# Performance work log

Measured on AMD Instinct MI355X. Metric: run time of the kernel, lower is better.

Reference implementation:

```python
import jax, jax.numpy as jnp
import numpy as np
import math

EMBED_DIM = 2048
NUM_HEADS = 16
HEAD_DIM = EMBED_DIM // NUM_HEADS
BATCH = 4
SEQ = 2048


def setup_inputs() -> dict:
    key = jax.random.key(0)
    ks = jax.random.split(key, 5)
    scale_qkv = 1.0 / math.sqrt(EMBED_DIM)
    x = jax.random.normal(ks[0], (BATCH, SEQ, EMBED_DIM), dtype=jnp.float32)
    w_qkv = jax.random.normal(ks[1], (3 * EMBED_DIM, EMBED_DIM), dtype=jnp.float32) * scale_qkv
    b_qkv = jnp.zeros((3 * EMBED_DIM,), dtype=jnp.float32)
    w_o = jax.random.normal(ks[2], (EMBED_DIM, EMBED_DIM), dtype=jnp.float32) * scale_qkv
    b_o = jnp.zeros((EMBED_DIM,), dtype=jnp.float32)
    return {"x": x, "w_qkv": w_qkv, "b_qkv": b_qkv, "w_o": w_o, "b_o": b_o}


def reference(x, w_qkv, b_qkv, w_o, b_o):
    B, S, D = x.shape
    # fused QKV projection: [B,S,3D]
    qkv = jnp.einsum('bsd,ed->bse', x, w_qkv) + b_qkv
    qkv = qkv.reshape(B, S, 3, NUM_HEADS, HEAD_DIM)
    qkv = jnp.transpose(qkv, (2, 0, 3, 1, 4))  # [3,B,H,S,hd]
    q, k, v = qkv[0], qkv[1], qkv[2]
    scores = jnp.einsum('bhqd,bhkd->bhqk', q, k) / math.sqrt(HEAD_DIM)
    probs = jax.nn.softmax(scores, axis=-1)
    out = jnp.einsum('bhqk,bhkd->bhqd', probs, v)
    out = jnp.transpose(out, (0, 2, 1, 3)).reshape(B, S, D)
    return jnp.einsum('bsd,ed->bse', out, w_o) + b_o
```

## Files before the change

kernel.cpp:

```cpp
#include <hip/hip_runtime.h>
#include <cstdint>
#include <cstddef>

typedef __attribute__((ext_vector_type(8))) __bf16 bf16x8;
typedef __attribute__((ext_vector_type(4))) float f32x4;
typedef __attribute__((ext_vector_type(4))) unsigned short u16x4;
typedef unsigned short u16;

#define BATCH 4
#define SEQ 2048
#define DIM 2048
#define NH 16
#define HD 128
#define BH (BATCH*NH)
#define MROWS (BATCH*SEQ)

__device__ static inline u16 f2bf(float f) {
  union { float f; uint32_t u; } v; v.f = f;
  uint32_t r = v.u + 0x7fffu + ((v.u >> 16) & 1u);
  return (u16)(r >> 16);
}

__device__ static inline uint32_t pkbf(float lo, float hi) {
  union { float f; uint32_t u; } a, b;
  a.f = lo; b.f = hi;
  return __builtin_amdgcn_perm(b.u + 0x8000u, a.u + 0x8000u, 0x07060302u);
}

__device__ static inline uint32_t cvtpk(float lo, float hi) {
  uint32_t r;
  asm("v_cvt_pk_bf16_f32 %0, %1, %2" : "=v"(r) : "v"(lo), "v"(hi));
  return r;
}

__device__ static inline void gload_lds16(const void* g, void* l) {
  __builtin_amdgcn_global_load_lds(
      (const __attribute__((address_space(1))) unsigned int*)g,
      (__attribute__((address_space(3))) unsigned int*)l, 16, 0, 0);
}

__device__ static inline f32x4 mfma_bf16(bf16x8 a, bf16x8 b, f32x4 c) {
  return __builtin_amdgcn_mfma_f32_16x16x32_bf16(a, b, c, 0, 0, 0);
}

#define NB_X   (MROWS * DIM / 1024)
#define NB_WQ  (3 * DIM * DIM / 1024)
#define NB_WO  (DIM * DIM / 1024)
#define NB_BIAS (3 * DIM / 256)
__global__ __launch_bounds__(256) void fused_cvt_kernel(
    const float4* __restrict__ x, u16x4* __restrict__ xb,
    const float4* __restrict__ wq, u16x4* __restrict__ wqb,
    const float4* __restrict__ wo, u16x4* __restrict__ wob,
    const float* __restrict__ bq, float* __restrict__ bqs, float scale2) {
  const int b = blockIdx.x;
  const int t = threadIdx.x;
  if (b < NB_X) {
    int i = b * 256 + t;
    float4 f = x[i];
    u16x4 o = { f2bf(f.x), f2bf(f.y), f2bf(f.z), f2bf(f.w) };
    xb[i] = o;
  } else if (b < NB_X + NB_WQ) {
    int i = (b - NB_X) * 256 + t;
    float4 f = wq[i];
    float s = (i < DIM * DIM / 4) ? scale2 : 1.0f;
    u16x4 o = { f2bf(f.x * s), f2bf(f.y * s), f2bf(f.z * s), f2bf(f.w * s) };
    wqb[i] = o;
  } else if (b < NB_X + NB_WQ + NB_WO) {
    int i = (b - NB_X - NB_WQ) * 256 + t;
    float4 f = wo[i];
    u16x4 o = { f2bf(f.x), f2bf(f.y), f2bf(f.z), f2bf(f.w) };
    wob[i] = o;
  } else {
    int i = (b - NB_X - NB_WQ - NB_WO) * 256 + t;
    bqs[i] = bq[i] * ((i < DIM) ? scale2 : 1.0f);
  }
}

__device__ __forceinline__ void ld_a(const char* sA, int wm, int ln, int quad,
                                     bf16x8 (&af)[4][2]) {
#pragma unroll
  for (int i = 0; i < 4; i++) {
    int r = wm * 64 + i * 16 + ln;
#pragma unroll
    for (int ks = 0; ks < 2; ks++) {
      int c = (ks * 4 + quad) ^ (r & 7);
      af[i][ks] = *(const bf16x8*)(sA + r * 128 + c * 16);
    }
  }
}

__device__ __forceinline__ void ld_b(const char* sB, int wn, int ln, int quad,
                                     bf16x8 (&bf)[2][2]) {
#pragma unroll
  for (int j = 0; j < 2; j++) {
    int r = wn * 32 + j * 16 + ln;
#pragma unroll
    for (int ks = 0; ks < 2; ks++) {
      int c = (ks * 4 + quad) ^ (r & 7);
      bf[j][ks] = *(const bf16x8*)(sB + r * 128 + c * 16);
    }
  }
}

template<int QM, int QN>
__device__ __forceinline__ void mm16(f32x4 (&acc)[8][4], const bf16x8 (&af)[4][2],
                                     const bf16x8 (&bf)[2][2]) {
  __builtin_amdgcn_s_setprio(1);
#pragma unroll
  for (int i = 0; i < 4; i++)
#pragma unroll
    for (int j = 0; j < 2; j++)
#pragma unroll
      for (int ks = 0; ks < 2; ks++)
        acc[QM * 4 + i][QN * 2 + j] =
            mfma_bf16(af[i][ks], bf[j][ks], acc[QM * 4 + i][QN * 2 + j]);
  __builtin_amdgcn_s_setprio(0);
}

template<int EPI>
__global__ __launch_bounds__(512, 2) void gemm_bt_kernel(
    const u16* __restrict__ A, const u16* __restrict__ W,
    const float* __restrict__ bias, float* __restrict__ Cout,
    int M, int N, int K,
    u16* __restrict__ qb, u16* __restrict__ kb, u16* __restrict__ vtb) {
  __shared__ __align__(16) char lds[131072];

  const int tid = threadIdx.x;
  const int wave = tid >> 6, lane = tid & 63;
  const int quad = lane >> 4, ln = lane & 15;
  const int wm = wave >> 2;
  const int wn = wave & 3;

  const int bid = blockIdx.x;
  const int c = bid & 7;
  const int u = bid >> 3;
  const int bx = u >> 2;
  const int by = c * 4 + (u & 3);
  const int mbase = by * 256;
  const int nbase = bx * 256;

  f32x4 acc[8][4];
#pragma unroll
  for (int i = 0; i < 8; i++)
#pragma unroll
    for (int j = 0; j < 4; j++) acc[i][j] = (f32x4){0.f, 0.f, 0.f, 0.f};

  const u16* gA[2][2];
  const u16* gB[2][2];
  int stOff0, stOff1;
  {
    stOff0 = (wave * 128 + lane) * 16;
    stOff1 = stOff0 + 1024;
#pragma unroll
    for (int s = 0; s < 2; s++) {
      int chunk = wave * 128 + s * 64 + lane;
      int r = chunk >> 3, sc = chunk & 7;
      int gc = sc ^ (r & 7);
#pragma unroll
      for (int g = 0; g < 2; g++) {
        int ra = (r >> 6) * 128 + g * 64 + (r & 63);
        gA[g][s] = A + (size_t)(mbase + ra) * K + gc * 8;
        int rb = (r >> 5) * 64 + g * 32 + (r & 31);
        gB[g][s] = W + (size_t)(nbase + rb) * K + gc * 8;
      }
    }
  }

  const int NT = K >> 6;
  const int NITER = NT >> 1;

#define SLOT_A(d, g) (lds + (((d) * 2 + (g)) << 14))
#define SLOT_B(d, g) (lds + 65536 + (((d) * 2 + (g)) << 14))
#define STAGE_A(d, t, g) do { char* sb_ = SLOT_A(d, g); \
    size_t ko_ = (size_t)((t) & (NT - 1)) * 64; \
    gload_lds16(gA[g][0] + ko_, sb_ + stOff0); \
    gload_lds16(gA[g][1] + ko_, sb_ + stOff1); } while (0)
#define STAGE_B(d, t, g) do { char* sb_ = SLOT_B(d, g); \
    size_t ko_ = (size_t)((t) & (NT - 1)) * 64; \
    gload_lds16(gB[g][0] + ko_, sb_ + stOff0); \
    gload_lds16(gB[g][1] + ko_, sb_ + stOff1); } while (0)
#define BAR  asm volatile("s_barrier" ::: "memory")
#define BARV asm volatile("s_waitcnt vmcnt(6)\n\ts_barrier" ::: "memory")

  STAGE_A(0, 0, 0); STAGE_B(0, 0, 0); STAGE_A(0, 0, 1); STAGE_B(0, 0, 1);
  STAGE_A(1, 1, 0); STAGE_B(1, 1, 0); STAGE_A(1, 1, 1);
  BARV;

  for (int it = 0; it < NITER; ++it) {
    const int t = it << 1;
    bf16x8 af[4][2], bq0[2][2], bq1[2][2];
    ld_a(SLOT_A(0, 0), wm, ln, quad, af);
    ld_b(SLOT_B(0, 0), wn, ln, quad, bq0);
    STAGE_B(1, t + 1, 1);
    mm16<0, 0>(acc, af, bq0); BAR;
    ld_b(SLOT_B(0, 1), wn, ln, quad, bq1);
    STAGE_A(0, t + 2, 0);
    mm16<0, 1>(acc, af, bq1); BAR;
    ld_a(SLOT_A(0, 1), wm, ln, quad, af);
    STAGE_B(0, t + 2, 0);
    mm16<1, 0>(acc, af, bq0); BAR;
    STAGE_A(0, t + 2, 1);
    mm16<1, 1>(acc, af, bq1); BARV;
    ld_a(SLOT_A(1, 0), wm, ln, quad, af);
    ld_b(SLOT_B(1, 0), wn, ln, quad, bq0);
    STAGE_B(0, t + 2, 1);
    mm16<0, 0>(acc, af, bq0); BAR;
    ld_b(SLOT_B(1, 1), wn, ln, quad, bq1);
    STAGE_A(1, t + 3, 0);
    mm16<0, 1>(acc, af, bq1); BAR;
    ld_a(SLOT_A(1, 1), wm, ln, quad, af);
    STAGE_B(1, t + 3, 0);
    mm16<1, 0>(acc, af, bq0); BAR;
    STAGE_A(1, t + 3, 1);
    mm16<1, 1>(acc, af, bq1); BARV;
  }
#undef SLOT_A
#undef SLOT_B
#undef STAGE_A
#undef STAGE_B
#undef BAR
#undef BARV

  if (EPI == 0 || (nbase >> 11) < 2) {
#pragma unroll
    for (int i = 0; i < 8; i++) {
#pragma unroll
      for (int j = 0; j < 4; j++) {
        int col = nbase + wn * 64 + j * 16 + ln;
        float bv = bias[col];
#pragma unroll
        for (int r = 0; r < 4; r++) {
          int row = mbase + wm * 128 + i * 16 + quad * 4 + r;
          float val = acc[i][j][r] + bv;
          if (EPI == 0) {
            Cout[(size_t)row * N + col] = val;
          } else {
            int b = row >> 11, s = row & 2047;
            int m3 = col >> 11, h = (col >> 7) & 15, d = col & 127;
            int bh = b * NH + h;
            u16 bfv = f2bf(val);
            if (m3 == 0) qb[((size_t)bh * SEQ + s) * HD + d] = bfv;
            else         kb[((size_t)bh * SEQ + s) * HD + d] = bfv;
          }
        }
      }
    }
  } else {
    asm volatile("s_waitcnt vmcnt(0)" ::: "memory");
    __syncthreads();
#pragma unroll
    for (int i = 0; i < 8; i++) {
      int rl0 = wm * 128 + i * 16 + quad * 4;
      int cs = rl0 >> 3;
      int half = (quad & 1);
#pragma unroll
      for (int j = 0; j < 4; j++) {
        int cl = wn * 64 + j * 16 + ln;
        float bv = bias[nbase + cl];
        uint2 w2;
        w2.x = pkbf(acc[i][j][0] + bv, acc[i][j][1] + bv);
        w2.y = pkbf(acc[i][j][2] + bv, acc[i][j][3] + bv);
        int cc = cs ^ (cl & 31);
        *(uint2*)(lds + cl * 512 + cc * 16 + half * 8) = w2;
      }
    }
    __syncthreads();
    u16* vdst = vtb + ((size_t)((mbase >> 11) * 2048 + (nbase & 2047))) * SEQ
                + (mbase & 2047);
#pragma unroll
    for (int rd = 0; rd < 16; rd++) {
      int idx = rd * 512 + tid;
      int cl = idx >> 5, cs = idx & 31;
      f32x4 v = *(const f32x4*)(lds + cl * 512 + ((cs ^ (cl & 31)) * 16));
      *(f32x4*)(vdst + (size_t)cl * SEQ + cs * 8) = v;
    }
  }
}

__global__ __launch_bounds__(256, 2) void attn_kernel(
    const u16* __restrict__ Q, const u16* __restrict__ Km,
    const u16* __restrict__ Vt, u16* __restrict__ Out) {
  __shared__ __align__(16) char lds[81920];
  char* ldsP = lds + 65536;

  const int tid = threadIdx.x;
  const int wave = tid >> 6, lane = tid & 63;
  const int quad = lane >> 4, ln = lane & 15;

  const int wg = blockIdx.x;
  const int swz = (wg & 7) * 128 + (wg >> 3);
  const int bh = swz >> 4;
  const int q0 = (swz & 15) * 128;

  const u16* Qb = Q + (size_t)bh * SEQ * HD;
  const u16* Kb = Km + (size_t)bh * SEQ * HD;
  const u16* Vb = Vt + (size_t)bh * HD * SEQ;

  bf16x8 qf[2][4];
#pragma unroll
  for (int nt = 0; nt < 2; nt++)
#pragma unroll
    for (int ks = 0; ks < 4; ks++) {
      int row = q0 + wave * 32 + nt * 16 + ln;
      qf[nt][ks] = *(const bf16x8*)(Qb + (size_t)row * HD + ks * 32 + quad * 8);
    }

  f32x4 oacc[8][2];
#pragma unroll
  for (int mt = 0; mt < 8; mt++)
#pragma unroll
    for (int nt = 0; nt < 2; nt++) oacc[mt][nt] = (f32x4){0.f, 0.f, 0.f, 0.f};
  float l_s[2] = {0.f, 0.f};

  char* Pw = ldsP + wave * 4096;

  const int chunk0 = wave * 256 + lane;
  const u16* gKp[4]; const u16* gVp[4]; int ldsOff[4];
#pragma unroll
  for (int s4 = 0; s4 < 4; s4++) {
    int chunk = chunk0 + s4 * 64;
    int rk = chunk >> 4, ck = chunk & 15;
    int gk = ck ^ (rk & 15);
    gKp[s4] = Kb + (size_t)rk * HD + gk * 8;
    int rv = chunk >> 3, cv = chunk & 7;
    int gv = cv ^ (rv & 7);
    gVp[s4] = Vb + (size_t)rv * SEQ + gv * 8;
    ldsOff[s4] = chunk * 16;
  }

#pragma unroll
  for (int s4 = 0; s4 < 4; s4++) {
    gload_lds16(gKp[s4], lds + ldsOff[s4]);
    gload_lds16(gVp[s4], lds + 16384 + ldsOff[s4]);
  }

  for (int kt = 0; kt < SEQ / 64; kt++) {
    {
      int t = (kt + 1) & (SEQ / 64 - 1);
      char* buf = lds + ((kt + 1) & 1) * 32768;
#pragma unroll
      for (int s4 = 0; s4 < 4; s4++) {
        gload_lds16(gKp[s4] + (size_t)t * 64 * HD, buf + ldsOff[s4]);
        gload_lds16(gVp[s4] + t * 64, buf + 16384 + ldsOff[s4]);
      }
    }
    asm volatile("s_waitcnt vmcnt(8)\n\ts_barrier" ::: "memory");

    const char* ldsK = lds + (kt & 1) * 32768;
    const char* ldsV = ldsK + 16384;

    f32x4 st[4][2];
#pragma unroll
    for (int mt = 0; mt < 4; mt++)
#pragma unroll
      for (int nt = 0; nt < 2; nt++) st[mt][nt] = (f32x4){0.f, 0.f, 0.f, 0.f};
    __builtin_amdgcn_s_setprio(1);
#pragma unroll
    for (int ks = 0; ks < 4; ks++) {
      bf16x8 kf[4];
#pragma unroll
      for (int mt = 0; mt < 4; mt++) {
        int row = mt * 16 + ln;
        int ch = (ks * 4 + quad) ^ (row & 15);
        kf[mt] = *(const bf16x8*)(ldsK + row * 256 + ch * 16);
      }
#pragma unroll
      for (int mt = 0; mt < 4; mt++)
#pragma unroll
        for (int nt = 0; nt < 2; nt++)
          st[mt][nt] = mfma_bf16(kf[mt], qf[nt][ks], st[mt][nt]);
    }
    __builtin_amdgcn_s_setprio(0);

#pragma unroll
    for (int nt = 0; nt < 2; nt++) {
      float lp = 0.f;
      u16* prow = (u16*)(Pw + (nt * 16 + ln) * 128);
#pragma unroll
      for (int mt = 0; mt < 4; mt++) {
        float p0 = __builtin_amdgcn_exp2f(st[mt][nt][0]);
        float p1 = __builtin_amdgcn_exp2f(st[mt][nt][1]);
        float p2 = __builtin_amdgcn_exp2f(st[mt][nt][2]);
        float p3 = __builtin_amdgcn_exp2f(st[mt][nt][3]);
        lp += (p0 + p1) + (p2 + p3);
        uint2 w2;
        w2.x = cvtpk(p0, p1);
        w2.y = cvtpk(p2, p3);
        int cc = (mt * 2 + (quad >> 1)) ^ (ln & 7);
        *(uint2*)((char*)prow + cc * 16 + (quad & 1) * 8) = w2;
      }
      l_s[nt] += lp;
    }
    asm volatile("s_waitcnt lgkmcnt(0)" ::: "memory");

    __builtin_amdgcn_s_setprio(1);
#pragma unroll
    for (int ks2 = 0; ks2 < 2; ks2++) {
      bf16x8 pb[2];
#pragma unroll
      for (int nt = 0; nt < 2; nt++) {
        int cc = (ks2 * 4 + quad) ^ (ln & 7);
        pb[nt] = *(const bf16x8*)(Pw + (nt * 16 + ln) * 128 + cc * 16);
      }
      bf16x8 vf[8];
#pragma unroll
      for (int mt = 0; mt < 8; mt++) {
        int row = mt * 16 + ln;
        int ch = (ks2 * 4 + quad) ^ (row & 7);
        vf[mt] = *(const bf16x8*)(ldsV + row * 128 + ch * 16);
      }
#pragma unroll
      for (int mt = 0; mt < 8; mt++)
#pragma unroll
        for (int nt = 0; nt < 2; nt++)
          oacc[mt][nt] = mfma_bf16(vf[mt], pb[nt], oacc[mt][nt]);
    }
    __builtin_amdgcn_s_setprio(0);
    asm volatile("s_waitcnt lgkmcnt(0)\n\ts_barrier" ::: "memory");
  }

  float inv[2];
#pragma unroll
  for (int nt = 0; nt < 2; nt++) {
    float l = l_s[nt];
    l += __shfl_xor(l, 16);
    l += __shfl_xor(l, 32);
    inv[nt] = 1.0f / l;
  }

  int b = bh >> 4, h = bh & 15;
#pragma unroll
  for (int nt = 0; nt < 2; nt++) {
    int srow = q0 + wave * 32 + nt * 16 + ln;
    size_t base = ((size_t)b * SEQ + srow) * DIM + h * HD;
#pragma unroll
    for (int mt = 0; mt < 8; mt++) {
      int d = mt * 16 + quad * 4;
      u16x4 o = { f2bf(oacc[mt][nt][0] * inv[nt]), f2bf(oacc[mt][nt][1] * inv[nt]),
                  f2bf(oacc[mt][nt][2] * inv[nt]), f2bf(oacc[mt][nt][3] * inv[nt]) };
      *(u16x4*)(Out + base + d) = o;
    }
  }
}

extern "C" void kernel_launch(void* const* d_in, const int* in_sizes, int n_in,
                              void* d_out, int out_size, void* d_ws, size_t ws_size,
                              hipStream_t stream) {
  const float* x     = (const float*)d_in[0];
  const float* w_qkv = (const float*)d_in[1];
  const float* b_qkv = (const float*)d_in[2];
  const float* w_o   = (const float*)d_in[3];
  const float* b_o   = (const float*)d_in[4];
  float* out = (float*)d_out;

  char* ws = (char*)d_ws;
  const size_t SZ_XBF  = (size_t)MROWS * DIM * 2;
  const size_t SZ_WQKV = (size_t)3 * DIM * DIM * 2;
  const size_t SZ_WO   = (size_t)DIM * DIM * 2;
  const size_t SZ_HEAD = (size_t)BH * SEQ * HD * 2;
  u16* x_bf    = (u16*)(ws);
  u16* wqkv_bf = (u16*)(ws + SZ_XBF);
  u16* wo_bf   = (u16*)(ws + SZ_XBF + SZ_WQKV);
  u16* qbuf    = (u16*)(ws + SZ_XBF + SZ_WQKV + SZ_WO);
  u16* kbuf    = (u16*)(ws + SZ_XBF + SZ_WQKV + SZ_WO + SZ_HEAD);
  u16* vtbuf   = (u16*)(ws + SZ_XBF + SZ_WQKV + SZ_WO + 2 * SZ_HEAD);
  float* bq_s  = (float*)(ws + SZ_XBF + SZ_WQKV + SZ_WO + 3 * SZ_HEAD);
  u16* attn_out = x_bf;

  (void)in_sizes; (void)n_in; (void)out_size; (void)ws_size;

  const float scale2 = (float)(0.08838834764831845 * 1.4426950408889634);

  fused_cvt_kernel<<<NB_X + NB_WQ + NB_WO + NB_BIAS, 256, 0, stream>>>(
      (const float4*)x, (u16x4*)x_bf,
      (const float4*)w_qkv, (u16x4*)wqkv_bf,
      (const float4*)w_o, (u16x4*)wo_bf,
      b_qkv, bq_s, scale2);

  gemm_bt_kernel<1><<<(3 * DIM / 256) * (MROWS / 256), 512, 0, stream>>>(
      x_bf, wqkv_bf, bq_s, nullptr, MROWS, 3 * DIM, DIM, qbuf, kbuf, vtbuf);

  attn_kernel<<<(SEQ / 128) * BH, 256, 0, stream>>>(
      qbuf, kbuf, vtbuf, attn_out);

  gemm_bt_kernel<0><<<(DIM / 256) * (MROWS / 256), 512, 0, stream>>>(
      attn_out, wo_bf, b_o, out, MROWS, DIM, DIM, nullptr, nullptr, nullptr);
}
```

Before: 518.4 us.

## Software-pipeline attention loop: overlap PV of previous tile with QK of current

Restructures the flash-attention inner loop so the P·V MFMAs for the previous key tile run after the current tile's QK^T and exp, with the V load for the next tile issued after the barrier. The intent is to let the exp/P-write latency overlap with matrix work and to remove the lgkmcnt wait between writing P and reading it back. It adds a loop epilogue and staggered K/V load timing. The vmcnt(8) wait count may no longer match the new load ordering, which risks correctness or extra stalls.

```diff
diff --git a/kernel.cpp b/kernel.cpp
--- a/kernel.cpp
+++ b/kernel.cpp
@@ -329,25 +329,22 @@
   }
 
 #pragma unroll
-  for (int s4 = 0; s4 < 4; s4++) {
-    gload_lds16(gKp[s4], lds + ldsOff[s4]);
-    gload_lds16(gVp[s4], lds + 16384 + ldsOff[s4]);
-  }
-
-  for (int kt = 0; kt < SEQ / 64; kt++) {
+  for (int s4 = 0; s4 < 4; s4++) gload_lds16(gKp[s4], lds + ldsOff[s4]);
+#pragma unroll
+  for (int s4 = 0; s4 < 4; s4++) gload_lds16(gVp[s4], lds + 16384 + ldsOff[s4]);
+
+  const int NTT = SEQ / 64;
+  for (int kt = 0; kt < NTT; kt++) {
     {
-      int t = (kt + 1) & (SEQ / 64 - 1);
+      int t = (kt + 1) & (NTT - 1);
       char* buf = lds + ((kt + 1) & 1) * 32768;
 #pragma unroll
-      for (int s4 = 0; s4 < 4; s4++) {
+      for (int s4 = 0; s4 < 4; s4++)
         gload_lds16(gKp[s4] + (size_t)t * 64 * HD, buf + ldsOff[s4]);
-        gload_lds16(gVp[s4] + t * 64, buf + 16384 + ldsOff[s4]);
-      }
     }
     asm volatile("s_waitcnt vmcnt(8)\n\ts_barrier" ::: "memory");
 
     const char* ldsK = lds + (kt & 1) * 32768;
-    const char* ldsV = ldsK + 16384;
 
     f32x4 st[4][2];
 #pragma unroll
@@ -371,6 +368,17 @@
           st[mt][nt] = mfma_bf16(kf[mt], qf[nt][ks], st[mt][nt]);
     }
     __builtin_amdgcn_s_setprio(0);
+
+    bf16x8 pb[2][2];
+    if (kt > 0) {
+#pragma unroll
+      for (int ks2 = 0; ks2 < 2; ks2++)
+#pragma unroll
+        for (int nt = 0; nt < 2; nt++) {
+          int cc = (ks2 * 4 + quad) ^ (ln & 7);
+          pb[ks2][nt] = *(const bf16x8*)(Pw + (nt * 16 + ln) * 128 + cc * 16);
+        }
+    }
 
 #pragma unroll
     for (int nt = 0; nt < 2; nt++) {
@@ -391,32 +399,67 @@
       }
       l_s[nt] += lp;
     }
-    asm volatile("s_waitcnt lgkmcnt(0)" ::: "memory");
-
-    __builtin_amdgcn_s_setprio(1);
-#pragma unroll
-    for (int ks2 = 0; ks2 < 2; ks2++) {
-      bf16x8 pb[2];
+
+    if (kt > 0) {
+      const char* ldsVp = lds + (((kt - 1) & 1) * 32768) + 16384;
+      __builtin_amdgcn_s_setprio(1);
+#pragma unroll
+      for (int ks2 = 0; ks2 < 2; ks2++) {
+        bf16x8 vf[8];
+#pragma unroll
+        for (int mt = 0; mt < 8; mt++) {
+          int row = mt * 16 + ln;
+          int ch = (ks2 * 4 + quad) ^ (row & 7);
+          vf[mt] = *(const bf16x8*)(ldsVp + row * 128 + ch * 16);
+        }
+#pragma unroll
+        for (int mt = 0; mt < 8; mt++)
+#pragma unroll
+          for (int nt = 0; nt < 2; nt++)
+            oacc[mt][nt] = mfma_bf16(vf[mt], pb[ks2][nt], oacc[mt][nt]);
+      }
+      __builtin_amdgcn_s_setprio(0);
+    }
+
+    asm volatile("s_waitcnt lgkmcnt(0)\n\ts_barrier" ::: "memory");
+
+    {
+      int t = (kt + 1) & (NTT - 1);
+      char* buf = lds + ((kt + 1) & 1) * 32768;
+#pragma unroll
+      for (int s4 = 0; s4 < 4; s4++)
+        gload_lds16(gVp[s4] + t * 64, buf + 16384 + ldsOff[s4]);
+    }
+  }
+
+  asm volatile("s_waitcnt vmcnt(8)\n\ts_barrier" ::: "memory");
+  {
+    bf16x8 pb[2][2];
+#pragma unroll
+    for (int ks2 = 0; ks2 < 2; ks2++)
 #pragma unroll
       for (int nt = 0; nt < 2; nt++) {
         int cc = (ks2 * 4 + quad) ^ (ln & 7);
-        pb[nt] = *(const bf16x8*)(Pw + (nt * 16 + ln) * 128 + cc * 16);
-      }
+        pb[ks2][nt] = *(const bf16x8*)(Pw + (nt * 16 + ln) * 128 + cc * 16);
+      }
+    const char* ldsVp = lds + (((NTT - 1) & 1) * 32768) + 16384;
+    __builtin_amdgcn_s_setprio(1);
+#pragma unroll
+    for (int ks2 = 0; ks2 < 2; ks2++) {
       bf16x8 vf[8];
 #pragma unroll
       for (int mt = 0; mt < 8; mt++) {
         int row = mt * 16 + ln;
         int ch = (ks2 * 4 + quad) ^ (row & 7);
-        vf[mt] = *(const bf16x8*)(ldsV + row * 128 + ch * 16);
+        vf[mt] = *(const bf16x8*)(ldsVp + row * 128 + ch * 16);
       }
 #pragma unroll
       for (int mt = 0; mt < 8; mt++)
 #pragma unroll
         for (int nt = 0; nt < 2; nt++)
-          oacc[mt][nt] = mfma_bf16(vf[mt], pb[nt], oacc[mt][nt]);
+          oacc[mt][nt] = mfma_bf16(vf[mt], pb[ks2][nt], oacc[mt][nt]);
     }
     __builtin_amdgcn_s_setprio(0);
-    asm volatile("s_waitcnt lgkmcnt(0)\n\ts_barrier" ::: "memory");
   }
 
   float inv[2];
```

Result: no change. 527.3 us (+1.7%).
